# Performance work log

Hardware: AMD Instinct MI355X
Metric: run time of the kernel (lower is better)

## Reference

```python
import jax, jax.numpy as jnp
import numpy as np

N = 400_000
E = 3_200_000
K = 5
H = 100
F_IN = 2
L = 5
BN_EPS = 1e-5


def setup_inputs() -> dict:
    key = jax.random.key(0)
    ks = jax.random.split(key, 6)
    x = jax.random.normal(ks[0], (N, F_IN), dtype=jnp.float32)
    edge_index = jax.random.randint(ks[1], (2, E), 0, N, dtype=jnp.int64)
    W0 = jax.random.normal(ks[2], (K, F_IN, H), dtype=jnp.float32) * 0.1
    b0 = jnp.zeros((H,), dtype=jnp.float32)
    Wr = jax.random.normal(ks[3], (L - 1, K, H, H), dtype=jnp.float32) * 0.1
    br = jnp.zeros((L - 1, H), dtype=jnp.float32)
    gamma = jnp.ones((L, H), dtype=jnp.float32)
    beta = jnp.zeros((L, H), dtype=jnp.float32)
    return {"x": x, "edge_index": edge_index, "W0": W0, "b0": b0,
            "Wr": Wr, "br": br, "gamma": gamma, "beta": beta}


def reference(x, edge_index, W0, b0, Wr, br, gamma, beta):
    n = x.shape[0]
    src, dst = edge_index[0], edge_index[1]

    # ChebConv normalization (lambda_max = 2, sym): L_hat = -D^{-1/2} A D^{-1/2}
    deg = jax.ops.segment_sum(jnp.ones(src.shape, jnp.float32), src, num_segments=n)
    dinv = jnp.where(deg > 0, jax.lax.rsqrt(jnp.maximum(deg, 1.0)), 0.0)
    norm = -dinv[src] * dinv[dst]  # [E]

    def prop(h):
        # out[i] = sum_{(j->i)} norm_e * h[j]
        return jax.ops.segment_sum(norm[:, None] * h[src], dst, num_segments=n)

    def cheb(h, W, b):
        # Chebyshev recurrence: T0 = h, T1 = L_hat h, Tk = 2 L_hat T_{k-1} - T_{k-2}
        Tx0 = h
        out = Tx0 @ W[0] + b
        Tx1 = prop(Tx0)
        out = out + Tx1 @ W[1]
        for k in range(2, W.shape[0]):
            Tx2 = 2.0 * prop(Tx1) - Tx0
            out = out + Tx2 @ W[k]
            Tx0, Tx1 = Tx1, Tx2
        return out

    def batch_norm(h, g, bt):
        m = h.mean(axis=0)
        v = h.var(axis=0)  # biased, as torch BN uses for normalization
        return g * (h - m) * jax.lax.rsqrt(v + BN_EPS) + bt

    h = x
    for layer in range(L):
        W = W0 if layer == 0 else Wr[layer - 1]
        b = b0 if layer == 0 else br[layer - 1]
        h = batch_norm(jax.nn.relu(cheb(h, W, b)), gamma[layer], beta[layer])
    return h
```

## Files before the change

### kernel.cpp

```cpp
#include <hip/hip_runtime.h>

#define H 100
#define FIN 2
#define KORD 5

typedef unsigned int uint32;
typedef unsigned short ushort16;
typedef __attribute__((ext_vector_type(8))) short s8v;
typedef __attribute__((ext_vector_type(4))) float f4v;

__device__ __forceinline__ ushort16 f2b(float x) {
  uint32 u = __float_as_uint(x);
  return (ushort16)((u + 0x7fffu + ((u >> 16) & 1u)) >> 16);
}
__device__ __forceinline__ float2 b2f2(uint32 v) {
  return make_float2(__uint_as_float(v << 16), __uint_as_float(v & 0xffff0000u));
}


__global__ __launch_bounds__(256) void deg_kernel(const int* __restrict__ src, const int* __restrict__ dst,
                                                  float* __restrict__ deg, int* __restrict__ indeg, int E) {
  int e = blockIdx.x * 256 + threadIdx.x;
  if (e < E) {
    atomicAdd(&deg[src[e]], 1.0f);
    atomicAdd(&indeg[dst[e]], 1);
  }
}

__global__ __launch_bounds__(256) void dinv_kernel(const float* __restrict__ deg, float* __restrict__ dinv, int n) {
  int i = blockIdx.x * 256 + threadIdx.x;
  if (i < n) {
    float d = deg[i];
    dinv[i] = d > 0.f ? rsqrtf(fmaxf(d, 1.f)) : 0.f;
  }
}

__global__ __launch_bounds__(256) void scan_block(const int* __restrict__ in, int* __restrict__ incl,
                                                  int* __restrict__ bsum, int n) {
  __shared__ int s[256];
  int i = blockIdx.x * 256 + threadIdx.x;
  int v = (i < n) ? in[i] : 0;
  s[threadIdx.x] = v;
  __syncthreads();
  for (int d = 1; d < 256; d <<= 1) {
    int t = (threadIdx.x >= d) ? s[threadIdx.x - d] : 0;
    __syncthreads();
    s[threadIdx.x] += t;
    __syncthreads();
  }
  if (i < n) incl[i] = s[threadIdx.x];
  if (threadIdx.x == 255) bsum[blockIdx.x] = s[255];
}

__global__ __launch_bounds__(256) void scan_sums(const int* __restrict__ bsum, int* __restrict__ bscan, int nb) {
  __shared__ int s[256];
  __shared__ int carry;
  if (threadIdx.x == 0) carry = 0;
  __syncthreads();
  for (int base = 0; base < nb; base += 256) {
    int i = base + threadIdx.x;
    int v = (i < nb) ? bsum[i] : 0;
    s[threadIdx.x] = v;
    __syncthreads();
    for (int d = 1; d < 256; d <<= 1) {
      int t = (threadIdx.x >= d) ? s[threadIdx.x - d] : 0;
      __syncthreads();
      s[threadIdx.x] += t;
      __syncthreads();
    }
    int c = carry;
    if (i < nb) bscan[i] = s[threadIdx.x] + c;
    __syncthreads();
    if (threadIdx.x == 0) carry = c + s[255];
    __syncthreads();
  }
}

__global__ __launch_bounds__(256) void finalize_offsets(const int* __restrict__ incl, const int* __restrict__ indeg,
                                                        const int* __restrict__ bscan, int* __restrict__ offsets,
                                                        int* __restrict__ cursor, int n, int total) {
  int i = blockIdx.x * 256 + threadIdx.x;
  if (i < n) {
    int prev = (blockIdx.x > 0) ? bscan[blockIdx.x - 1] : 0;
    int excl = incl[i] - indeg[i] + prev;
    offsets[i] = excl;
    cursor[i] = excl;
  }
  if (i == 0) offsets[n] = total;
}

__global__ __launch_bounds__(256) void build_csr(const int* __restrict__ src, const int* __restrict__ dst,
                                                 const float* __restrict__ dinv, int* __restrict__ cursor,
                                                 int2* __restrict__ csr, int E) {
  int e = blockIdx.x * 256 + threadIdx.x;
  if (e < E) {
    int s = src[e], d = dst[e];
    float nrm = -dinv[s] * dinv[d];
    int p = atomicAdd(&cursor[d], 1);
    csr[p] = make_int2(s, __float_as_int(nrm));
  }
}

__global__ __launch_bounds__(256) void pad_zero(uint4* __restrict__ b, int nrows) {
  int i = blockIdx.x * 256 + threadIdx.x;
  if (i < nrows * 4) {
    uint4 z; z.x = 0; z.y = 0; z.z = 0; z.w = 0;
    b[(size_t)(i >> 2) * 16 + 12 + (i & 3)] = z;
  }
}


__global__ __launch_bounds__(256) void prop2(const float* __restrict__ h, const float* __restrict__ prev,
                                             float* __restrict__ out, const int* __restrict__ offs,
                                             const int2* __restrict__ csr, int n, int mode) {
  int i = blockIdx.x * 256 + threadIdx.x;
  if (i >= n) return;
  float a0 = 0.f, a1 = 0.f;
  int e0 = offs[i], e1 = offs[i + 1];
  int e = e0;
  for (; e + 4 <= e1; e += 4) {
    int2 c0 = csr[e], c1 = csr[e + 1], c2 = csr[e + 2], c3 = csr[e + 3];
    float w0 = __int_as_float(c0.y), w1 = __int_as_float(c1.y);
    float w2 = __int_as_float(c2.y), w3 = __int_as_float(c3.y);
    float x0 = h[2 * c0.x], y0 = h[2 * c0.x + 1];
    float x1 = h[2 * c1.x], y1 = h[2 * c1.x + 1];
    float x2 = h[2 * c2.x], y2 = h[2 * c2.x + 1];
    float x3 = h[2 * c3.x], y3 = h[2 * c3.x + 1];
    a0 = fmaf(w0, x0, a0); a1 = fmaf(w0, y0, a1);
    a0 = fmaf(w1, x1, a0); a1 = fmaf(w1, y1, a1);
    a0 = fmaf(w2, x2, a0); a1 = fmaf(w2, y2, a1);
    a0 = fmaf(w3, x3, a0); a1 = fmaf(w3, y3, a1);
  }
  for (; e < e1; ++e) {
    int2 c = csr[e];
    float w = __int_as_float(c.y);
    a0 = fmaf(w, h[2 * c.x], a0);
    a1 = fmaf(w, h[2 * c.x + 1], a1);
  }
  if (mode) {
    a0 = 2.f * a0 - prev[2 * i];
    a1 = 2.f * a1 - prev[2 * i + 1];
  }
  out[2 * i] = a0;
  out[2 * i + 1] = a1;
}

__global__ __launch_bounds__(256) void prop_hb(const uint32* __restrict__ h, const uint32* __restrict__ prev,
                                               uint32* __restrict__ out, const int* __restrict__ offs,
                                               const int2* __restrict__ csr, int n, int mode) {
  int lane = threadIdx.x & 63;
  int node = blockIdx.x * 4 + (threadIdx.x >> 6);
  if (node >= n) return;
  int grp = lane >> 4, sub = lane & 15;
  int e0 = offs[node], e1 = offs[node + 1];
  const uint4* hq = (const uint4*)h;

  float a[8];
#pragma unroll
  for (int j = 0; j < 8; ++j) a[j] = 0.f;

  for (int base = e0; base < e1; base += 64) {
    int mm = e1 - base;
    int2 cv = make_int2(0, 0);
    if (lane < mm) cv = csr[base + lane];
    int lim = mm < 64 ? mm : 64;
    int nr = (lim + 7) >> 3;
    for (int r = 0; r < nr; ++r) {
      int ea = 8 * r + grp;
      int sa = __shfl(cv.x, ea);
      float wa = __int_as_float(__shfl(cv.y, ea));
      int sb = __shfl(cv.x, ea + 4);
      float wb = __int_as_float(__shfl(cv.y, ea + 4));
      uint4 va = hq[(size_t)sa * 16 + sub];
      uint4 vb = hq[(size_t)sb * 16 + sub];
      float2 f;
      f = b2f2(va.x); a[0] = fmaf(wa, f.x, a[0]); a[1] = fmaf(wa, f.y, a[1]);
      f = b2f2(va.y); a[2] = fmaf(wa, f.x, a[2]); a[3] = fmaf(wa, f.y, a[3]);
      f = b2f2(va.z); a[4] = fmaf(wa, f.x, a[4]); a[5] = fmaf(wa, f.y, a[5]);
      f = b2f2(va.w); a[6] = fmaf(wa, f.x, a[6]); a[7] = fmaf(wa, f.y, a[7]);
      f = b2f2(vb.x); a[0] = fmaf(wb, f.x, a[0]); a[1] = fmaf(wb, f.y, a[1]);
      f = b2f2(vb.y); a[2] = fmaf(wb, f.x, a[2]); a[3] = fmaf(wb, f.y, a[3]);
      f = b2f2(vb.z); a[4] = fmaf(wb, f.x, a[4]); a[5] = fmaf(wb, f.y, a[5]);
      f = b2f2(vb.w); a[6] = fmaf(wb, f.x, a[6]); a[7] = fmaf(wb, f.y, a[7]);
    }
  }

#pragma unroll
  for (int j = 0; j < 8; ++j) a[j] += __shfl_xor(a[j], 16);
#pragma unroll
  for (int j = 0; j < 8; ++j) a[j] += __shfl_xor(a[j], 32);

  if (grp != 0) return;
  uint4* oq = (uint4*)out;
  size_t qi = (size_t)node * 16 + sub;
  if (sub >= 13) {
    uint4 z; z.x = 0; z.y = 0; z.z = 0; z.w = 0;
    oq[qi] = z;
    return;
  }
  if (sub == 12) { a[4] = 0.f; a[5] = 0.f; a[6] = 0.f; a[7] = 0.f; }
  float rr[8];
  if (mode) {
    uint4 pv = ((const uint4*)prev)[qi];
    float2 p;
    p = b2f2(pv.x); rr[0] = 2.f * a[0] - p.x; rr[1] = 2.f * a[1] - p.y;
    p = b2f2(pv.y); rr[2] = 2.f * a[2] - p.x; rr[3] = 2.f * a[3] - p.y;
    p = b2f2(pv.z); rr[4] = 2.f * a[4] - p.x; rr[5] = 2.f * a[5] - p.y;
    p = b2f2(pv.w); rr[6] = 2.f * a[6] - p.x; rr[7] = 2.f * a[7] - p.y;
  } else {
#pragma unroll
    for (int j = 0; j < 8; ++j) rr[j] = a[j];
  }
  uint4 pk;
  pk.x = (uint32)f2b(rr[0]) | ((uint32)f2b(rr[1]) << 16);
  pk.y = (uint32)f2b(rr[2]) | ((uint32)f2b(rr[3]) << 16);
  pk.z = (uint32)f2b(rr[4]) | ((uint32)f2b(rr[5]) << 16);
  pk.w = (uint32)f2b(rr[6]) | ((uint32)f2b(rr[7]) << 16);
  oq[qi] = pk;
}


__global__ __launch_bounds__(64) void wconv(const float* __restrict__ Wr, ushort16* __restrict__ Wf) {
  int b = blockIdx.x;
  int l = threadIdx.x;
  int mat = b / 28, rem = b % 28;
  int kc = rem / 7, ft = rem % 7;
  const float* Wm = Wr + (size_t)mat * H * H;
  int c0 = kc * 32 + (l >> 4) * 8;
  int f = ft * 16 + (l & 15);
  ushort16 vals[8];
#pragma unroll
  for (int j = 0; j < 8; ++j) {
    int c = c0 + j;
    float v = (c < H && f < H) ? Wm[c * H + f] : 0.f;
    vals[j] = f2b(v);
  }
  uint4 pk;
  pk.x = (uint32)vals[0] | ((uint32)vals[1] << 16);
  pk.y = (uint32)vals[2] | ((uint32)vals[3] << 16);
  pk.z = (uint32)vals[4] | ((uint32)vals[5] << 16);
  pk.w = (uint32)vals[6] | ((uint32)vals[7] << 16);
  *(uint4*)(Wf + (size_t)b * 512 + l * 8) = pk;
}


__global__ __launch_bounds__(256) void gemm_mfma(const ushort16* __restrict__ Ta, const ushort16* __restrict__ Tb,
                                                 const ushort16* __restrict__ Tc, int nk,
                                                 const ushort16* __restrict__ Wf, const float* __restrict__ bias,
                                                 float* __restrict__ C, int n, int initMode) {
  int t = threadIdx.x;
  int w = t >> 6, l = t & 63;
  int ml = l & 15, quad = l >> 4;
  int n0 = blockIdx.x * 128 + 32 * w;

  f4v acc[2][7];
  if (initMode) {
#pragma unroll
    for (int ft = 0; ft < 7; ++ft) {
      int f = ft * 16 + ml;
      float b = (f < H) ? bias[f] : 0.f;
      f4v v = {b, b, b, b};
      acc[0][ft] = v;
      acc[1][ft] = v;
    }
  } else {
#pragma unroll
    for (int s = 0; s < 2; ++s)
#pragma unroll
      for (int ft = 0; ft < 7; ++ft) {
        int f = ft * 16 + ml;
#pragma unroll
        for (int r = 0; r < 4; ++r) {
          int row = n0 + 16 * s + quad * 4 + r;
          acc[s][ft][r] = (f < H && row < n) ? C[(size_t)row * H + f] : 0.f;
        }
      }
  }

  for (int k = 0; k < nk; ++k) {
    const ushort16* T = (k == 0) ? Ta : ((k == 1) ? Tb : Tc);
#pragma unroll
    for (int kc = 0; kc < 4; ++kc) {
      s8v bfrag[7];
      const ushort16* wb = Wf + ((size_t)(k * 4 + kc) * 7) * 512 + l * 8;
#pragma unroll
      for (int ft = 0; ft < 7; ++ft) bfrag[ft] = *(const s8v*)(wb + ft * 512);
#pragma unroll
      for (int s = 0; s < 2; ++s) {
        const ushort16* ap = T + (size_t)(n0 + 16 * s + ml) * 128 + kc * 32 + quad * 8;
        s8v a = *(const s8v*)ap;
#pragma unroll
        for (int ft = 0; ft < 7; ++ft)
          acc[s][ft] = __builtin_amdgcn_mfma_f32_16x16x32_bf16(a, bfrag[ft], acc[s][ft], 0, 0, 0);
      }
    }
  }

#pragma unroll
  for (int s = 0; s < 2; ++s)
#pragma unroll
    for (int ft = 0; ft < 7; ++ft) {
      int f = ft * 16 + ml;
      if (f < H) {
#pragma unroll
        for (int r = 0; r < 4; ++r) {
          int row = n0 + 16 * s + quad * 4 + r;
          if (row < n) C[(size_t)row * H + f] = acc[s][ft][r];
        }
      }
    }
}


__global__ __launch_bounds__(128) void layer0_out(const float* __restrict__ x, const float* __restrict__ t1,
                                                  const float* __restrict__ t2, const float* __restrict__ t3,
                                                  const float* __restrict__ t4, const float* __restrict__ W0,
                                                  const float* __restrict__ b0, float* __restrict__ C, int n) {
  int f = threadIdx.x;
  bool act = f < H;
  float w[10];
  float b = 0.f;
  if (act) {
#pragma unroll
    for (int j = 0; j < 10; ++j) w[j] = W0[j * H + f];
    b = b0[f];
  }
  int n0 = blockIdx.x * 32;
  int n1 = n0 + 32 < n ? n0 + 32 : n;
  for (int i = n0; i < n1; ++i) {
    if (!act) continue;
    float acc = b;
    acc = fmaf(x[2 * i],      w[0], acc);
    acc = fmaf(x[2 * i + 1],  w[1], acc);
    acc = fmaf(t1[2 * i],     w[2], acc);
    acc = fmaf(t1[2 * i + 1], w[3], acc);
    acc = fmaf(t2[2 * i],     w[4], acc);
    acc = fmaf(t2[2 * i + 1], w[5], acc);
    acc = fmaf(t3[2 * i],     w[6], acc);
    acc = fmaf(t3[2 * i + 1], w[7], acc);
    acc = fmaf(t4[2 * i],     w[8], acc);
    acc = fmaf(t4[2 * i + 1], w[9], acc);
    C[(size_t)i * H + f] = acc;
  }
}


__global__ __launch_bounds__(128) void bn_stats(const float* __restrict__ acc, float* __restrict__ stats, int n) {
  int f = threadIdx.x;
  int n0 = blockIdx.x * 512;
  int n1 = n0 + 512 < n ? n0 + 512 : n;
  if (f < H) {
    float s = 0.f, s2 = 0.f;
    for (int i = n0; i < n1; ++i) {
      float v = fmaxf(acc[(size_t)i * H + f], 0.f);
      s += v;
      s2 = fmaf(v, v, s2);
    }
    atomicAdd(&stats[f], s);
    atomicAdd(&stats[128 + f], s2);
  }
}

__global__ __launch_bounds__(128) void bn_params(float* __restrict__ stats, const float* __restrict__ gamma,
                                                 const float* __restrict__ beta, int n) {
  int f = threadIdx.x;
  if (f >= H) return;
  float inv_n = 1.f / (float)n;
  float m = stats[f] * inv_n;
  float v = stats[128 + f] * inv_n - m * m;
  float is = rsqrtf(v + 1e-5f);
  float g = gamma[f] * is;
  stats[256 + f] = g;
  stats[384 + f] = beta[f] - m * g;
}

__global__ __launch_bounds__(256) void bn_final(const float* __restrict__ acc, const float* __restrict__ mi,
                                                float* __restrict__ out, int total) {
  int idx = blockIdx.x * 256 + threadIdx.x;
  if (idx >= total) return;
  int f = idx % H;
  float v = fmaxf(acc[idx], 0.f);
  out[idx] = fmaf(v, mi[f], mi[128 + f]);
}

__global__ __launch_bounds__(256) void bn_final_bf16(const float* __restrict__ acc, const float* __restrict__ mi,
                                                     ushort16* __restrict__ out, int total) {
  int idx = blockIdx.x * 256 + threadIdx.x;
  if (idx >= total) return;
  int row = idx / H, f = idx - row * H;
  float v = fmaxf(acc[idx], 0.f);
  out[(size_t)row * 128 + f] = f2b(fmaf(v, mi[f], mi[128 + f]));
}


extern "C" void kernel_launch(void* const* d_in, const int* in_sizes, int n_in,
                              void* d_out, int out_size, void* d_ws, size_t ws_size,
                              hipStream_t stream) {
  const float* x     = (const float*)d_in[0];
  const int*   ei    = (const int*)d_in[1];
  const float* W0    = (const float*)d_in[2];
  const float* b0    = (const float*)d_in[3];
  const float* Wr    = (const float*)d_in[4];
  const float* br    = (const float*)d_in[5];
  const float* gamma = (const float*)d_in[6];
  const float* beta  = (const float*)d_in[7];
  float* C = (float*)d_out;

  const int N = in_sizes[0] / FIN;
  const int E = in_sizes[1] / 2;
  const int* src = ei;
  const int* dst = ei + E;

  char* ws = (char*)d_ws;
  size_t off = 0;
  auto alloc = [&](size_t bytes) -> void* {
    void* p = ws + off;
    off = (off + bytes + 255) & ~(size_t)255;
    return p;
  };

  size_t TB = (size_t)N * 128 * sizeof(ushort16);
  ushort16* B0     = (ushort16*)alloc(TB);
  ushort16* B1     = (ushort16*)alloc(TB);
  ushort16* B2     = (ushort16*)alloc(TB);
  ushort16* Wf     = (ushort16*)alloc((size_t)20 * 14336 * sizeof(ushort16));
  float* t1       = (float*)alloc((size_t)N * 2 * 4);
  float* t2       = (float*)alloc((size_t)N * 2 * 4);
  float* t3       = (float*)alloc((size_t)N * 2 * 4);
  float* t4       = (float*)alloc((size_t)N * 2 * 4);
  float* deg      = (float*)alloc((size_t)N * 4);
  int*   indeg    = (int*)alloc((size_t)N * 4);
  float* dinv     = (float*)alloc((size_t)N * 4);
  int*   incl     = (int*)alloc((size_t)N * 4);
  int*   bsum     = (int*)alloc(8192 * 4);
  int*   bscan    = (int*)alloc(8192 * 4);
  int*   offsets  = (int*)alloc((size_t)(N + 1) * 4);
  int*   cursor   = (int*)alloc((size_t)N * 4);
  int2*  csr      = (int2*)alloc((size_t)E * 8);
  float* stats    = (float*)alloc(512 * 4);

  int gE = (E + 255) / 256;
  int gN = (N + 255) / 256;

  hipMemsetAsync(deg, 0, (size_t)N * 4, stream);
  hipMemsetAsync(indeg, 0, (size_t)N * 4, stream);

  deg_kernel<<<gE, 256, 0, stream>>>(src, dst, deg, indeg, E);
  dinv_kernel<<<gN, 256, 0, stream>>>(deg, dinv, N);
  scan_block<<<gN, 256, 0, stream>>>(indeg, incl, bsum, N);
  scan_sums<<<1, 256, 0, stream>>>(bsum, bscan, gN);
  finalize_offsets<<<gN, 256, 0, stream>>>(incl, indeg, bscan, offsets, cursor, N, E);
  build_csr<<<gE, 256, 0, stream>>>(src, dst, dinv, cursor, csr, E);
  wconv<<<20 * 28, 64, 0, stream>>>(Wr, Wf);
  pad_zero<<<(N * 4 + 255) / 256, 256, 0, stream>>>((uint4*)B0, N);

  prop2<<<gN, 256, 0, stream>>>(x,  x,  t1, offsets, csr, N, 0);
  prop2<<<gN, 256, 0, stream>>>(t1, x,  t2, offsets, csr, N, 1);
  prop2<<<gN, 256, 0, stream>>>(t2, t1, t3, offsets, csr, N, 1);
  prop2<<<gN, 256, 0, stream>>>(t3, t2, t4, offsets, csr, N, 1);
  layer0_out<<<(N + 31) / 32, 128, 0, stream>>>(x, t1, t2, t3, t4, W0, b0, C, N);
  hipMemsetAsync(stats, 0, 1024, stream);
  bn_stats<<<(N + 511) / 512, 128, 0, stream>>>(C, stats, N);
  bn_params<<<1, 128, 0, stream>>>(stats, gamma, beta, N);
  bn_final_bf16<<<(N * H + 255) / 256, 256, 0, stream>>>(C, stats + 256, B0, N * H);

  int gG = (N + 127) / 128;
  int gP = (N + 3) / 4;
  for (int layer = 1; layer < 5; ++layer) {
    const ushort16* WfL = Wf + (size_t)(layer - 1) * 5 * 14336;
    const float* bl = br + (size_t)(layer - 1) * H;
    prop_hb<<<gP, 256, 0, stream>>>((const uint32*)B0, (const uint32*)B0, (uint32*)B1, offsets, csr, N, 0);
    prop_hb<<<gP, 256, 0, stream>>>((const uint32*)B1, (const uint32*)B0, (uint32*)B2, offsets, csr, N, 1);
    gemm_mfma<<<gG, 256, 0, stream>>>(B0, B1, B2, 3, WfL, bl, C, N, 1);
    prop_hb<<<gP, 256, 0, stream>>>((const uint32*)B2, (const uint32*)B1, (uint32*)B0, offsets, csr, N, 1);
    prop_hb<<<gP, 256, 0, stream>>>((const uint32*)B0, (const uint32*)B2, (uint32*)B1, offsets, csr, N, 1);
    gemm_mfma<<<gG, 256, 0, stream>>>(B0, B1, B0, 2, WfL + (size_t)3 * 14336, bl, C, N, 0);
    hipMemsetAsync(stats, 0, 1024, stream);
    bn_stats<<<(N + 511) / 512, 128, 0, stream>>>(C, stats, N);
    bn_params<<<1, 128, 0, stream>>>(stats, gamma + (size_t)layer * H, beta + (size_t)layer * H, N);
    if (layer < 4)
      bn_final_bf16<<<(N * H + 255) / 256, 256, 0, stream>>>(C, stats + 256, B0, N * H);
    else
      bn_final<<<(N * H + 255) / 256, 256, 0, stream>>>(C, stats + 256, C, N * H);
  }
}
```

Measured before the change: 5.820 ms.

## Stage CSR edges in LDS per 64-node block and fuse GEMMs into one

The propagation kernel now gives each block 64 destination nodes (16 per wave). It loads the block's edge range of the CSR into shared memory and reads indices and weights from LDS instead of shuffling them per node. If the range exceeds the LDS capacity it falls back to direct global loads. When workspace allows, two extra basis buffers are allocated so all five Chebyshev terms stay live and a single GEMM consumes them, instead of two GEMMs with a read-modify-write of the fp32 output. The trade-offs are longer per-block serial work, which may lower parallelism, and higher workspace use.

```diff
diff --git a/kernel.cpp b/kernel.cpp
--- a/kernel.cpp
+++ b/kernel.cpp
@@ -3,6 +3,8 @@
 #define H 100
 #define FIN 2
 #define KORD 5
+#define NPB 64
+#define SE_CAP 2048
 
 typedef unsigned int uint32;
 typedef unsigned short ushort16;
@@ -15,6 +17,13 @@
 }
 __device__ __forceinline__ float2 b2f2(uint32 v) {
   return make_float2(__uint_as_float(v << 16), __uint_as_float(v & 0xffff0000u));
+}
+__device__ __forceinline__ void acc8(float* a, uint4 v, float w) {
+  float2 f;
+  f = b2f2(v.x); a[0] = fmaf(w, f.x, a[0]); a[1] = fmaf(w, f.y, a[1]);
+  f = b2f2(v.y); a[2] = fmaf(w, f.x, a[2]); a[3] = fmaf(w, f.y, a[3]);
+  f = b2f2(v.z); a[4] = fmaf(w, f.x, a[4]); a[5] = fmaf(w, f.y, a[5]);
+  f = b2f2(v.w); a[6] = fmaf(w, f.x, a[6]); a[7] = fmaf(w, f.y, a[7]);
 }
 
 
@@ -145,78 +154,100 @@
   out[2 * i + 1] = a1;
 }
 
-__global__ __launch_bounds__(256) void prop_hb(const uint32* __restrict__ h, const uint32* __restrict__ prev,
-                                               uint32* __restrict__ out, const int* __restrict__ offs,
-                                               const int2* __restrict__ csr, int n, int mode) {
-  int lane = threadIdx.x & 63;
-  int node = blockIdx.x * 4 + (threadIdx.x >> 6);
-  if (node >= n) return;
-  int grp = lane >> 4, sub = lane & 15;
-  int e0 = offs[node], e1 = offs[node + 1];
+__global__ __launch_bounds__(256) void prop_hb2(const uint32* __restrict__ h, const uint32* __restrict__ prev,
+                                                uint32* __restrict__ out, const int* __restrict__ offs,
+                                                const int2* __restrict__ csr, int n, int mode) {
+  __shared__ int2 se[SE_CAP];
+  __shared__ int soff[NPB + 1];
+  int t = threadIdx.x;
+  int n0 = blockIdx.x * NPB;
+  if (t <= NPB) {
+    int idx = n0 + t;
+    soff[t] = offs[idx < n ? idx : n];
+  }
+  __syncthreads();
+  int e0b = soff[0], e1b = soff[NPB];
+  bool staged = (e1b - e0b) <= SE_CAP;
+  if (staged) {
+    for (int i = e0b + t; i < e1b; i += 256) se[i - e0b] = csr[i];
+  }
+  __syncthreads();
+
+  int w = t >> 6, lane = t & 63, grp = lane >> 4, sub = lane & 15;
   const uint4* hq = (const uint4*)h;
-
-  float a[8];
-#pragma unroll
-  for (int j = 0; j < 8; ++j) a[j] = 0.f;
-
-  for (int base = e0; base < e1; base += 64) {
-    int mm = e1 - base;
-    int2 cv = make_int2(0, 0);
-    if (lane < mm) cv = csr[base + lane];
-    int lim = mm < 64 ? mm : 64;
-    int nr = (lim + 7) >> 3;
-    for (int r = 0; r < nr; ++r) {
-      int ea = 8 * r + grp;
-      int sa = __shfl(cv.x, ea);
-      float wa = __int_as_float(__shfl(cv.y, ea));
-      int sb = __shfl(cv.x, ea + 4);
-      float wb = __int_as_float(__shfl(cv.y, ea + 4));
-      uint4 va = hq[(size_t)sa * 16 + sub];
-      uint4 vb = hq[(size_t)sb * 16 + sub];
-      float2 f;
-      f = b2f2(va.x); a[0] = fmaf(wa, f.x, a[0]); a[1] = fmaf(wa, f.y, a[1]);
-      f = b2f2(va.y); a[2] = fmaf(wa, f.x, a[2]); a[3] = fmaf(wa, f.y, a[3]);
-      f = b2f2(va.z); a[4] = fmaf(wa, f.x, a[4]); a[5] = fmaf(wa, f.y, a[5]);
-      f = b2f2(va.w); a[6] = fmaf(wa, f.x, a[6]); a[7] = fmaf(wa, f.y, a[7]);
-      f = b2f2(vb.x); a[0] = fmaf(wb, f.x, a[0]); a[1] = fmaf(wb, f.y, a[1]);
-      f = b2f2(vb.y); a[2] = fmaf(wb, f.x, a[2]); a[3] = fmaf(wb, f.y, a[3]);
-      f = b2f2(vb.z); a[4] = fmaf(wb, f.x, a[4]); a[5] = fmaf(wb, f.y, a[5]);
-      f = b2f2(vb.w); a[6] = fmaf(wb, f.x, a[6]); a[7] = fmaf(wb, f.y, a[7]);
-    }
-  }
-
-#pragma unroll
-  for (int j = 0; j < 8; ++j) a[j] += __shfl_xor(a[j], 16);
-#pragma unroll
-  for (int j = 0; j < 8; ++j) a[j] += __shfl_xor(a[j], 32);
-
-  if (grp != 0) return;
   uint4* oq = (uint4*)out;
-  size_t qi = (size_t)node * 16 + sub;
-  if (sub >= 13) {
-    uint4 z; z.x = 0; z.y = 0; z.z = 0; z.w = 0;
-    oq[qi] = z;
-    return;
-  }
-  if (sub == 12) { a[4] = 0.f; a[5] = 0.f; a[6] = 0.f; a[7] = 0.f; }
-  float rr[8];
-  if (mode) {
-    uint4 pv = ((const uint4*)prev)[qi];
-    float2 p;
-    p = b2f2(pv.x); rr[0] = 2.f * a[0] - p.x; rr[1] = 2.f * a[1] - p.y;
-    p = b2f2(pv.y); rr[2] = 2.f * a[2] - p.x; rr[3] = 2.f * a[3] - p.y;
-    p = b2f2(pv.z); rr[4] = 2.f * a[4] - p.x; rr[5] = 2.f * a[5] - p.y;
-    p = b2f2(pv.w); rr[6] = 2.f * a[6] - p.x; rr[7] = 2.f * a[7] - p.y;
-  } else {
-#pragma unroll
-    for (int j = 0; j < 8; ++j) rr[j] = a[j];
-  }
-  uint4 pk;
-  pk.x = (uint32)f2b(rr[0]) | ((uint32)f2b(rr[1]) << 16);
-  pk.y = (uint32)f2b(rr[2]) | ((uint32)f2b(rr[3]) << 16);
-  pk.z = (uint32)f2b(rr[4]) | ((uint32)f2b(rr[5]) << 16);
-  pk.w = (uint32)f2b(rr[6]) | ((uint32)f2b(rr[7]) << 16);
-  oq[qi] = pk;
+  bool wr = (grp == 0);
+
+  for (int ni = 0; ni < 16; ++ni) {
+    int node = n0 + w * 16 + ni;
+    if (node >= n) break;
+    int li = w * 16 + ni;
+    int e0 = soff[li], e1 = soff[li + 1];
+    int deg = e1 - e0;
+    size_t qi = (size_t)node * 16 + sub;
+
+    uint4 pv; pv.x = 0; pv.y = 0; pv.z = 0; pv.w = 0;
+    if (mode && wr && sub < 13) pv = ((const uint4*)prev)[qi];
+
+    float a[8];
+#pragma unroll
+    for (int j = 0; j < 8; ++j) a[j] = 0.f;
+
+    int nr = (deg + 7) >> 3;
+    if (staged) {
+      int eb = e0 - e0b;
+      for (int r = 0; r < nr; ++r) {
+        int ea = 8 * r + grp;
+        int2 ca = (ea < deg) ? se[eb + ea] : make_int2(0, 0);
+        int2 cb = (ea + 4 < deg) ? se[eb + ea + 4] : make_int2(0, 0);
+        uint4 va = hq[(size_t)ca.x * 16 + sub];
+        uint4 vb = hq[(size_t)cb.x * 16 + sub];
+        acc8(a, va, __int_as_float(ca.y));
+        acc8(a, vb, __int_as_float(cb.y));
+      }
+    } else {
+      const int2* cp = csr + e0;
+      for (int r = 0; r < nr; ++r) {
+        int ea = 8 * r + grp;
+        int2 ca = (ea < deg) ? cp[ea] : make_int2(0, 0);
+        int2 cb = (ea + 4 < deg) ? cp[ea + 4] : make_int2(0, 0);
+        uint4 va = hq[(size_t)ca.x * 16 + sub];
+        uint4 vb = hq[(size_t)cb.x * 16 + sub];
+        acc8(a, va, __int_as_float(ca.y));
+        acc8(a, vb, __int_as_float(cb.y));
+      }
+    }
+
+#pragma unroll
+    for (int j = 0; j < 8; ++j) a[j] += __shfl_xor(a[j], 16);
+#pragma unroll
+    for (int j = 0; j < 8; ++j) a[j] += __shfl_xor(a[j], 32);
+
+    if (!wr) continue;
+    if (sub >= 13) {
+      uint4 z; z.x = 0; z.y = 0; z.z = 0; z.w = 0;
+      oq[qi] = z;
+      continue;
+    }
+    if (sub == 12) { a[4] = 0.f; a[5] = 0.f; a[6] = 0.f; a[7] = 0.f; }
+    float rr[8];
+    if (mode) {
+      float2 p;
+      p = b2f2(pv.x); rr[0] = 2.f * a[0] - p.x; rr[1] = 2.f * a[1] - p.y;
+      p = b2f2(pv.y); rr[2] = 2.f * a[2] - p.x; rr[3] = 2.f * a[3] - p.y;
+      p = b2f2(pv.z); rr[4] = 2.f * a[4] - p.x; rr[5] = 2.f * a[5] - p.y;
+      p = b2f2(pv.w); rr[6] = 2.f * a[6] - p.x; rr[7] = 2.f * a[7] - p.y;
+    } else {
+#pragma unroll
+      for (int j = 0; j < 8; ++j) rr[j] = a[j];
+    }
+    uint4 pk;
+    pk.x = (uint32)f2b(rr[0]) | ((uint32)f2b(rr[1]) << 16);
+    pk.y = (uint32)f2b(rr[2]) | ((uint32)f2b(rr[3]) << 16);
+    pk.z = (uint32)f2b(rr[4]) | ((uint32)f2b(rr[5]) << 16);
+    pk.w = (uint32)f2b(rr[6]) | ((uint32)f2b(rr[7]) << 16);
+    oq[qi] = pk;
+  }
 }
 
 
@@ -245,7 +276,8 @@
 
 
 __global__ __launch_bounds__(256) void gemm_mfma(const ushort16* __restrict__ Ta, const ushort16* __restrict__ Tb,
-                                                 const ushort16* __restrict__ Tc, int nk,
+                                                 const ushort16* __restrict__ Tc, const ushort16* __restrict__ Td,
+                                                 const ushort16* __restrict__ Te, int nk,
                                                  const ushort16* __restrict__ Wf, const float* __restrict__ bias,
                                                  float* __restrict__ C, int n, int initMode) {
   int t = threadIdx.x;
@@ -278,7 +310,7 @@
   }
 
   for (int k = 0; k < nk; ++k) {
-    const ushort16* T = (k == 0) ? Ta : ((k == 1) ? Tb : Tc);
+    const ushort16* T = (k == 0) ? Ta : (k == 1) ? Tb : (k == 2) ? Tc : (k == 3) ? Td : Te;
 #pragma unroll
     for (int kc = 0; kc < 4; ++kc) {
       s8v bfrag[7];
@@ -439,6 +471,14 @@
   int2*  csr      = (int2*)alloc((size_t)E * 8);
   float* stats    = (float*)alloc(512 * 4);
 
+  ushort16* B3 = B0;
+  ushort16* B4 = B1;
+  bool five = (off + 2 * TB + 512 <= ws_size);
+  if (five) {
+    B3 = (ushort16*)alloc(TB);
+    B4 = (ushort16*)alloc(TB);
+  }
+
   int gE = (E + 255) / 256;
   int gN = (N + 255) / 256;
 
@@ -465,16 +505,24 @@
   bn_final_bf16<<<(N * H + 255) / 256, 256, 0, stream>>>(C, stats + 256, B0, N * H);
 
   int gG = (N + 127) / 128;
-  int gP = (N + 3) / 4;
+  int gP = (N + NPB - 1) / NPB;
   for (int layer = 1; layer < 5; ++layer) {
     const ushort16* WfL = Wf + (size_t)(layer - 1) * 5 * 14336;
     const float* bl = br + (size_t)(layer - 1) * H;
-    prop_hb<<<gP, 256, 0, stream>>>((const uint32*)B0, (const uint32*)B0, (uint32*)B1, offsets, csr, N, 0);
-    prop_hb<<<gP, 256, 0, stream>>>((const uint32*)B1, (const uint32*)B0, (uint32*)B2, offsets, csr, N, 1);
-    gemm_mfma<<<gG, 256, 0, stream>>>(B0, B1, B2, 3, WfL, bl, C, N, 1);
-    prop_hb<<<gP, 256, 0, stream>>>((const uint32*)B2, (const uint32*)B1, (uint32*)B0, offsets, csr, N, 1);
-    prop_hb<<<gP, 256, 0, stream>>>((const uint32*)B0, (const uint32*)B2, (uint32*)B1, offsets, csr, N, 1);
-    gemm_mfma<<<gG, 256, 0, stream>>>(B0, B1, B0, 2, WfL + (size_t)3 * 14336, bl, C, N, 0);
+    if (five) {
+      prop_hb2<<<gP, 256, 0, stream>>>((const uint32*)B0, (const uint32*)B0, (uint32*)B1, offsets, csr, N, 0);
+      prop_hb2<<<gP, 256, 0, stream>>>((const uint32*)B1, (const uint32*)B0, (uint32*)B2, offsets, csr, N, 1);
+      prop_hb2<<<gP, 256, 0, stream>>>((const uint32*)B2, (const uint32*)B1, (uint32*)B3, offsets, csr, N, 1);
+      prop_hb2<<<gP, 256, 0, stream>>>((const uint32*)B3, (const uint32*)B2, (uint32*)B4, offsets, csr, N, 1);
+      gemm_mfma<<<gG, 256, 0, stream>>>(B0, B1, B2, B3, B4, 5, WfL, bl, C, N, 1);
+    } else {
+      prop_hb2<<<gP, 256, 0, stream>>>((const uint32*)B0, (const uint32*)B0, (uint32*)B1, offsets, csr, N, 0);
+      prop_hb2<<<gP, 256, 0, stream>>>((const uint32*)B1, (const uint32*)B0, (uint32*)B2, offsets, csr, N, 1);
+      gemm_mfma<<<gG, 256, 0, stream>>>(B0, B1, B2, B0, B1, 3, WfL, bl, C, N, 1);
+      prop_hb2<<<gP, 256, 0, stream>>>((const uint32*)B2, (const uint32*)B1, (uint32*)B0, offsets, csr, N, 1);
+      prop_hb2<<<gP, 256, 0, stream>>>((const uint32*)B0, (const uint32*)B2, (uint32*)B1, offsets, csr, N, 1);
+      gemm_mfma<<<gG, 256, 0, stream>>>(B0, B1, B0, B0, B1, 2, WfL + (size_t)3 * 14336, bl, C, N, 0);
+    }
     hipMemsetAsync(stats, 0, 1024, stream);
     bn_stats<<<(N + 511) / 512, 128, 0, stream>>>(C, stats, N);
     bn_params<<<1, 128, 0, stream>>>(stats, gamma + (size_t)layer * H, beta + (size_t)layer * H, N);
```

New measurement: 5.221 ms. -10.3%, faster.
